# Kernel optimization log

Measured on AMD Instinct MI355X. Metric: run time of the kernel, lower is better.

The kernel has to match this reference:

```python
import jax, jax.numpy as jnp
import numpy as np

B, L, T = 32, 512, 48
START_ID, END_ID = 46, 47


def setup_inputs() -> dict:
    key = jax.random.key(0)
    kf, kt, ks = jax.random.split(key, 3)
    features = jax.random.normal(kf, (B, L, T), dtype=jnp.float32)
    transitions = jax.random.normal(kt, (T, T), dtype=jnp.float32) * 0.1
    seqLens = jax.random.randint(ks, (B,), 1, L + 1)  # lengths in [1, L]
    mask = jnp.arange(L)[None, :] < seqLens[:, None]  # [B, L] bool
    return {"features": features, "transitions": transitions,
            "seqLens": seqLens, "mask": mask}


def reference(features, transitions, seqLens, mask):
    # features: [B, L, T]; transitions: [T, T]
    Bv, Lv, Tv = features.shape
    # scores[b, t, i, j] = transitions[i, j] + features[b, t, i]
    scores = transitions[None, None, :, :] + features[:, :, :, None]  # [B,L,T,T]

    alpha0 = scores[:, 0, :, START_ID]  # [B, T] = trans[:, start] + feat[:, 0, :]

    def step(alpha_prev, s_t):
        # alpha_t[b, i] = logsumexp_j( alpha_{t-1}[b, j] + s_t[b, i, j] )
        a = jax.nn.logsumexp(alpha_prev[:, None, :] + s_t, axis=2)
        return a, a

    scores_t = jnp.swapaxes(scores, 0, 1)  # [L, B, T, T]
    _, alphas_rest = jax.lax.scan(step, alpha0, scores_t[1:])  # [L-1, B, T]
    alpha = jnp.concatenate([alpha0[None], alphas_rest], axis=0)  # [L, B, T]
    alpha = jnp.swapaxes(alpha, 0, 1)  # [B, L, T]

    # gather alpha at position seqLens-1 per batch element
    last = jnp.take_along_axis(alpha, (seqLens - 1)[:, None, None], axis=1)[:, 0, :]  # [B,T]
    last = last + transitions[END_ID][None, :]
    logZ = jnp.sum(jax.nn.logsumexp(last, axis=1))  # scalar
    return logZ, scores
```

## Files before the change

kernel.cpp:

```cpp
#include <hip/hip_runtime.h>

#define BB 32
#define LL 512
#define TT 48
#define START_ID 46
#define END_ID 47

constexpr int   BLT  = BB * LL * TT;
constexpr unsigned NSC = 37748736u;
constexpr unsigned NGRP = 9437183u;

constexpr int SEGS   = 31;
constexpr int SEGLEN = 16;
constexpr int GW     = 1152;
constexpr int NSEG   = BB * SEGS;
constexpr int SOFF   = NSEG * GW;
constexpr int ZOFF   = SOFF + NSEG;
constexpr int ZFOFF  = ZOFF + 32;
constexpr size_t WS_NEED = (size_t)(ZFOFF + 32) * 4;

typedef __fp16 f16x2 __attribute__((ext_vector_type(2)));
typedef __fp16 f16x8 __attribute__((ext_vector_type(8)));
typedef float  f32x4 __attribute__((ext_vector_type(4)));
typedef unsigned u32x4 __attribute__((ext_vector_type(4)));

__device__ __forceinline__ float fexp2(float x) { return __builtin_amdgcn_exp2f(x); }
__device__ __forceinline__ float flog2(float x) { return __builtin_amdgcn_logf(x); }
__device__ __forceinline__ float rfirst(float x) {
  return __uint_as_float(__builtin_amdgcn_readfirstlane(__float_as_uint(x)));
}
__device__ __forceinline__ float fdot2(f16x2 a, f16x2 b, float c) {
  return __builtin_amdgcn_fdot2(a, b, c, false);
}
__device__ __forceinline__ f16x2 bc(unsigned u) { return __builtin_bit_cast(f16x2, u); }
__device__ __forceinline__ unsigned pk2(float a, float b) {
  return __builtin_bit_cast(unsigned, __builtin_amdgcn_cvt_pkrtz(a, b));
}
__device__ __forceinline__ float dpp_xor1(float x) {
  return __int_as_float(__builtin_amdgcn_update_dpp(
      __float_as_int(x), __float_as_int(x), 0xB1, 0xF, 0xF, true));
}
__device__ __forceinline__ f16x8 b8(unsigned d0, unsigned d1) {
  u32x4 u; u.x = d0; u.y = d1; u.z = 0u; u.w = 0u;
  return __builtin_bit_cast(f16x8, u);
}
__device__ __forceinline__ f32x4 MF(f16x8 a, f16x8 b, f32x4 c) {
  return __builtin_amdgcn_mfma_f32_16x16x32_f16(a, b, c, 0, 0, 0);
}
__device__ __forceinline__ unsigned magicv(unsigned i) {
  return 0x5EC0DE5Au + i * 2654435761u;
}

#define GLD16(gp, lp)                                                        \
  __builtin_amdgcn_global_load_lds(                                          \
      (const __attribute__((address_space(1))) unsigned int*)(gp),           \
      (__attribute__((address_space(3))) unsigned int*)(lp), 16, 0, 0)

__device__ __attribute__((noinline)) void crf_tree_body(
    const float* __restrict__ feat, const float* __restrict__ trans,
    float* __restrict__ ws, float* lds, int wg, int lane)
{
  constexpr float LOG2E = 1.4426950408889634f;
  unsigned* gws = (unsigned*)ws;
  const int b  = wg / SEGS, s = wg - b * SEGS;
  const int col = lane & 15, grp = lane >> 4, rb = grp * 4;

  const char* gbase = (const char*)feat + (size_t)b * 98304 + (size_t)(SEGLEN * s + 1) * 192;
#pragma unroll
  for (int w = 0; w < 3; ++w)
    GLD16(gbase + w * 1024 + lane * 16, (char*)lds + w * 1024);

  float4 T_[3][3];
#pragma unroll
  for (int I = 0; I < 3; ++I)
#pragma unroll
    for (int K = 0; K < 3; ++K) {
      const float4 t4 = *(const float4*)(trans + (I * 16 + col) * 48 + K * 16 + rb);
      T_[I][K].x = fexp2(t4.x * LOG2E);
      T_[I][K].y = fexp2(t4.y * LOG2E);
      T_[I][K].z = fexp2(t4.z * LOG2E);
      T_[I][K].w = fexp2(t4.w * LOG2E);
    }

  unsigned Bd[3][3][2];
#pragma unroll
  for (int K = 0; K < 3; ++K)
#pragma unroll
    for (int J = 0; J < 3; ++J) {
      const float b0 = (K == J && rb + 0 == col) ? 1.f : 0.f;
      const float b1 = (K == J && rb + 1 == col) ? 1.f : 0.f;
      const float b2 = (K == J && rb + 2 == col) ? 1.f : 0.f;
      const float b3 = (K == J && rb + 3 == col) ? 1.f : 0.f;
      Bd[K][J][0] = pk2(b0, b1);
      Bd[K][J][1] = pk2(b2, b3);
    }

  asm volatile("s_waitcnt vmcnt(0)" ::: "memory");
  __builtin_amdgcn_sched_barrier(0);

  float km = 0.f, Sacc = 0.f;
  f32x4 C[3][3];
  const f32x4 zz = {0.f, 0.f, 0.f, 0.f};

  for (int p = 0; p < SEGLEN; ++p) {
    Sacc += km;
    float ef[3];
    ef[0] = fexp2(fmaf(lds[p * 48 +  0 + col], LOG2E, -km));
    ef[1] = fexp2(fmaf(lds[p * 48 + 16 + col], LOG2E, -km));
    ef[2] = fexp2(fmaf(lds[p * 48 + 32 + col], LOG2E, -km));
    f16x8 A_[3][3];
#pragma unroll
    for (int I = 0; I < 3; ++I)
#pragma unroll
      for (int K = 0; K < 3; ++K) {
        u32x4 u;
        u.x = pk2(T_[I][K].x * ef[I], T_[I][K].y * ef[I]);
        u.y = pk2(T_[I][K].z * ef[I], T_[I][K].w * ef[I]);
        u.z = 0u; u.w = 0u;
        A_[I][K] = __builtin_bit_cast(f16x8, u);
      }
#pragma unroll
    for (int I = 0; I < 3; ++I)
#pragma unroll
      for (int J = 0; J < 3; ++J) {
        f32x4 c = MF(A_[I][0], b8(Bd[0][J][0], Bd[0][J][1]), zz);
        c = MF(A_[I][1], b8(Bd[1][J][0], Bd[1][J][1]), c);
        c = MF(A_[I][2], b8(Bd[2][J][0], Bd[2][J][1]), c);
        C[I][J] = c;
      }
    const unsigned u00 = __builtin_amdgcn_readfirstlane(__float_as_uint(C[0][0][0]));
    km = (float)((int)((u00 >> 23) & 255u) - 127);
#pragma unroll
    for (int K = 0; K < 3; ++K)
#pragma unroll
      for (int J = 0; J < 3; ++J) {
        Bd[K][J][0] = pk2(C[K][J][0], C[K][J][1]);
        Bd[K][J][1] = pk2(C[K][J][2], C[K][J][3]);
      }
  }

  const unsigned gb = (unsigned)wg * GW;
#pragma unroll
  for (int I = 0; I < 3; ++I)
#pragma unroll
    for (int J = 0; J < 3; ++J)
#pragma unroll
      for (int r = 0; r < 4; ++r) {
        const float cn = dpp_xor1(C[I][J][r]);
        const unsigned pk = pk2(C[I][J][r], cn);
        if (!(col & 1))
          gws[gb + (unsigned)((I * 16 + rb + r) * 24 + ((J * 16 + col) >> 1))] = pk;
      }
  if (lane == 0) ws[SOFF + wg] = Sacc;
}

__global__ __launch_bounds__(64) void crf_tree_kernel(
    const float* __restrict__ feat, const float* __restrict__ trans,
    float* __restrict__ ws)
{
  __shared__ __align__(16) float fls[SEGLEN * 48];
  crf_tree_body(feat, trans, ws, fls, blockIdx.x, threadIdx.x);
}

__device__ __attribute__((noinline)) void crf_phaseB(
    const float* __restrict__ feat, const float* __restrict__ trans,
    const int* __restrict__ seqLens, float* __restrict__ ws, int b, int lane)
{
  constexpr float LOG2E = 1.4426950408889634f;
  constexpr float LN2   = 0.6931471805599453f;
  const unsigned* gws = (const unsigned*)ws;
  const int ii = lane < 47 ? lane : 47;
  const int Lb = seqLens[b];
  const int steps = Lb - 1;
  const int nfull = steps >> 4;

  f16x2 E00,E01,E02,E03,E04,E05,E06,E07,E08,E09,E10,E11,
        E12,E13,E14,E15,E16,E17,E18,E19,E20,E21,E22,E23;
#define LDE(V, J) { const float e0_ = fexp2(trans[ii*48 + 2*(J)]     * LOG2E); \
                    const float e1_ = fexp2(trans[ii*48 + 2*(J) + 1] * LOG2E); \
                    V = __builtin_amdgcn_cvt_pkrtz(e0_, e1_); }
  LDE(E00,0)  LDE(E01,1)  LDE(E02,2)  LDE(E03,3)  LDE(E04,4)  LDE(E05,5)
  LDE(E06,6)  LDE(E07,7)  LDE(E08,8)  LDE(E09,9)  LDE(E10,10) LDE(E11,11)
  LDE(E12,12) LDE(E13,13) LDE(E14,14) LDE(E15,15) LDE(E16,16) LDE(E17,17)
  LDE(E18,18) LDE(E19,19) LDE(E20,20) LDE(E21,21) LDE(E22,22) LDE(E23,23)
#undef LDE
  const float tS = trans[ii * 48 + START_ID];
  const float tE = trans[END_ID * 48 + ii];
  const float* fb = feat + (size_t)b * (LL * TT);

  const float a0 = (tS + fb[ii]) * LOG2E;
  const float anch = rfirst(a0);
  float v = fexp2(a0 - anch);
  float sigma = anch;

#define RL24                                                               \
        unsigned s00,s01,s02,s03,s04,s05,s06,s07,s08,s09,s10,s11,          \
                 s12,s13,s14,s15,s16,s17,s18,s19,s20,s21,s22,s23;          \
        s00=__builtin_amdgcn_readlane(pku,0);  s01=__builtin_amdgcn_readlane(pku,2);  \
        s02=__builtin_amdgcn_readlane(pku,4);  s03=__builtin_amdgcn_readlane(pku,6);  \
        s04=__builtin_amdgcn_readlane(pku,8);  s05=__builtin_amdgcn_readlane(pku,10); \
        s06=__builtin_amdgcn_readlane(pku,12); s07=__builtin_amdgcn_readlane(pku,14); \
        s08=__builtin_amdgcn_readlane(pku,16); s09=__builtin_amdgcn_readlane(pku,18); \
        s10=__builtin_amdgcn_readlane(pku,20); s11=__builtin_amdgcn_readlane(pku,22); \
        s12=__builtin_amdgcn_readlane(pku,24); s13=__builtin_amdgcn_readlane(pku,26); \
        s14=__builtin_amdgcn_readlane(pku,28); s15=__builtin_amdgcn_readlane(pku,30); \
        s16=__builtin_amdgcn_readlane(pku,32); s17=__builtin_amdgcn_readlane(pku,34); \
        s18=__builtin_amdgcn_readlane(pku,36); s19=__builtin_amdgcn_readlane(pku,38); \
        s20=__builtin_amdgcn_readlane(pku,40); s21=__builtin_amdgcn_readlane(pku,42); \
        s22=__builtin_amdgcn_readlane(pku,44); s23=__builtin_amdgcn_readlane(pku,46);

  const unsigned* grow = gws + (size_t)(b * SEGS) * GW + ii * 24;
  u32x4 h0,h1,h2,h3,h4,h5, n0,n1,n2,n3,n4,n5;
  if (nfull > 0) {
    const u32x4* gp = (const u32x4*)grow;
    h0 = gp[0]; h1 = gp[1]; h2 = gp[2]; h3 = gp[3]; h4 = gp[4]; h5 = gp[5];
  }
  for (int s = 0; s < nfull; ++s) {
    if (s + 1 < nfull) {
      const u32x4* gp = (const u32x4*)(grow + (size_t)(s + 1) * GW);
      n0 = gp[0]; n1 = gp[1]; n2 = gp[2]; n3 = gp[3]; n4 = gp[4]; n5 = gp[5];
    }
    const float pn = dpp_xor1(v);
    const unsigned pku = pk2(v, pn);
    RL24
    float d0, d1, d2, d3;
    d0 = fdot2(bc(h0.x), bc(s00), 0.0f);
    d1 = fdot2(bc(h0.y), bc(s01), 0.0f);
    d2 = fdot2(bc(h0.z), bc(s02), 0.0f);
    d3 = fdot2(bc(h0.w), bc(s03), 0.0f);
    d0 = fdot2(bc(h1.x), bc(s04), d0);
    d1 = fdot2(bc(h1.y), bc(s05), d1);
    d2 = fdot2(bc(h1.z), bc(s06), d2);
    d3 = fdot2(bc(h1.w), bc(s07), d3);
    d0 = fdot2(bc(h2.x), bc(s08), d0);
    d1 = fdot2(bc(h2.y), bc(s09), d1);
    d2 = fdot2(bc(h2.z), bc(s10), d2);
    d3 = fdot2(bc(h2.w), bc(s11), d3);
    d0 = fdot2(bc(h3.x), bc(s12), d0);
    d1 = fdot2(bc(h3.y), bc(s13), d1);
    d2 = fdot2(bc(h3.z), bc(s14), d2);
    d3 = fdot2(bc(h3.w), bc(s15), d3);
    d0 = fdot2(bc(h4.x), bc(s16), d0);
    d1 = fdot2(bc(h4.y), bc(s17), d1);
    d2 = fdot2(bc(h4.z), bc(s18), d2);
    d3 = fdot2(bc(h4.w), bc(s19), d3);
    d0 = fdot2(bc(h5.x), bc(s20), d0);
    d1 = fdot2(bc(h5.y), bc(s21), d1);
    d2 = fdot2(bc(h5.z), bc(s22), d2);
    d3 = fdot2(bc(h5.w), bc(s23), d3);
    const float dot = (d0 + d1) + (d2 + d3);
    const unsigned ub = __builtin_amdgcn_readfirstlane(__float_as_uint(dot));
    const int e = (int)((ub >> 23) & 255u) - 127;
    v = dot * __uint_as_float((unsigned)(127 - e) << 23);
    sigma += (float)e + ws[SOFF + b * SEGS + s];
    h0 = n0; h1 = n1; h2 = n2; h3 = n3; h4 = n4; h5 = n5;
  }

  int t = nfull * 16 + 1;
  if (t <= steps) {
    float f_cur = fb[(size_t)t * 48 + ii];
    for (; t <= steps; ++t) {
      const int tn = (t + 1 <= steps) ? t + 1 : t;
      const float f_nxt = fb[(size_t)tn * 48 + ii];
      const float pn = dpp_xor1(v);
      const unsigned pku = pk2(v, pn);
      RL24
      float d0, d1, d2, d3;
      d0 = fdot2(E00, bc(s00), 0.0f);
      d1 = fdot2(E01, bc(s01), 0.0f);
      d2 = fdot2(E02, bc(s02), 0.0f);
      d3 = fdot2(E03, bc(s03), 0.0f);
      d0 = fdot2(E04, bc(s04), d0);
      d1 = fdot2(E05, bc(s05), d1);
      d2 = fdot2(E06, bc(s06), d2);
      d3 = fdot2(E07, bc(s07), d3);
      d0 = fdot2(E08, bc(s08), d0);
      d1 = fdot2(E09, bc(s09), d1);
      d2 = fdot2(E10, bc(s10), d2);
      d3 = fdot2(E11, bc(s11), d3);
      d0 = fdot2(E12, bc(s12), d0);
      d1 = fdot2(E13, bc(s13), d1);
      d2 = fdot2(E14, bc(s14), d2);
      d3 = fdot2(E15, bc(s15), d3);
      d0 = fdot2(E16, bc(s16), d0);
      d1 = fdot2(E17, bc(s17), d1);
      d2 = fdot2(E18, bc(s18), d2);
      d3 = fdot2(E19, bc(s19), d3);
      d0 = fdot2(E20, bc(s20), d0);
      d1 = fdot2(E21, bc(s21), d1);
      d2 = fdot2(E22, bc(s22), d2);
      d3 = fdot2(E23, bc(s23), d3);
      const float dot = (d0 + d1) + (d2 + d3);
      const float w = dot * fexp2(f_cur * LOG2E);
      const unsigned ub = __builtin_amdgcn_readfirstlane(__float_as_uint(w));
      const int e = (int)((ub >> 23) & 255u) - 127;
      v = w * __uint_as_float((unsigned)(127 - e) << 23);
      sigma += (float)e;
      f_cur = f_nxt;
    }
  }
#undef RL24

  float contrib = (lane < 48) ? v * fexp2(tE * LOG2E) : 0.0f;
#pragma unroll
  for (int off = 32; off; off >>= 1) contrib += __shfl_xor(contrib, off, 64);
  if (lane == 0) ws[ZOFF + b] = (flog2(contrib) + sigma) * LN2;
  __threadfence();
  if (lane == 0)
    __hip_atomic_store((unsigned*)ws + ZFOFF + b, magicv((unsigned)(NSEG + b)),
                       __ATOMIC_RELAXED, __HIP_MEMORY_SCOPE_AGENT);
}

__device__ __forceinline__ void scores_writer_rng(
    const float* __restrict__ feat, float* __restrict__ out,
    float* lds, unsigned k, unsigned kstride, unsigned kend)
{
  for (; k < kend; k += kstride) {
    const unsigned idx = 3u + 4u * k;
    const unsigned r0 = idx / 48u;
    const unsigned j0 = idx - r0 * 48u;
    const unsigned i0 = r0 % 48u;
    const unsigned rn = (r0 + 1u < (unsigned)BLT) ? r0 + 1u : (unsigned)(BLT - 1);
    const float fa = feat[r0];
    const float fn = feat[rn];
    const unsigned i1 = (i0 + 1u < 48u) ? i0 + 1u : 0u;
    float v[4];
#pragma unroll
    for (int e = 0; e < 4; ++e) {
      const unsigned j = j0 + (unsigned)e;
      const bool wr = j >= 48u;
      const unsigned jj = wr ? j - 48u : j;
      v[e] = (wr ? fn : fa) + lds[(wr ? i1 : i0) * 48u + jj];
    }
    float4 o; o.x = v[0]; o.y = v[1]; o.z = v[2]; o.w = v[3];
    *(float4*)(out + 4u + 4u * (size_t)k) = o;
  }
}

__global__ __launch_bounds__(256) void crf_fusedB_kernel(
    const float* __restrict__ feat, const float* __restrict__ trans,
    const int* __restrict__ seqLens, float* __restrict__ out,
    float* __restrict__ ws)
{
  __shared__ __align__(16) float lds[2304];
  const int blk = blockIdx.x;
  const int tid = threadIdx.x;

  if (blk < BB) {
    const int b = blk;
    if (tid >= 64) {
      if (b == 0) {
        if (tid <= 66) out[tid - 63] = feat[0] + trans[tid - 64];
        else if (tid == 67) out[NSC] = feat[BLT - 1] + trans[2303];
      }
      return;
    }
    crf_phaseB(feat, trans, seqLens, ws, b, tid);
    if (b == 0) {
      const unsigned* zf = (const unsigned*)ws + ZFOFF;
      if (tid > 0 && tid < 32) {
        const unsigned want = magicv((unsigned)(NSEG + tid));
        while (__hip_atomic_load(zf + tid, __ATOMIC_RELAXED, __HIP_MEMORY_SCOPE_AGENT) != want)
          __builtin_amdgcn_s_sleep(2);
      }
      __threadfence();
      float v = (tid < 32) ? ws[ZOFF + tid] : 0.0f;
#pragma unroll
      for (int off = 32; off; off >>= 1) v += __shfl_xor(v, off, 64);
      if (tid == 0) out[0] = v;
    }
    return;
  }

  for (int s = tid; s < 2304; s += 256) lds[s] = trans[s];
  __syncthreads();
  scores_writer_rng(feat, out, lds,
                    (unsigned)(blk - BB) * 256u + tid,
                    (gridDim.x - BB) * 256u, NGRP);
}

__device__ __attribute__((noinline)) void crf_recursion_body(
    const float* __restrict__ feat, const float* __restrict__ trans,
    const int* __restrict__ seqLens, float* __restrict__ ws,
    float* lds, int blk, int lane)
{
  constexpr float LOG2E = 1.4426950408889634f;
  const int ii = lane < 47 ? lane : 47;
  const char* gbase = (const char*)(feat + (size_t)blk * (LL * TT));
  const int Lb = seqLens[blk];

#pragma unroll
  for (int w = 0; w < 6; ++w)
    GLD16(gbase + w * 1024 + lane * 16, (char*)&lds[0] + w * 1024);

  f16x2 E00,E01,E02,E03,E04,E05,E06,E07,E08,E09,E10,E11,
        E12,E13,E14,E15,E16,E17,E18,E19,E20,E21,E22,E23;
#define LDE(V, J) { const float e0_ = fexp2(trans[ii*48 + 2*(J)]     * LOG2E); \
                    const float e1_ = fexp2(trans[ii*48 + 2*(J) + 1] * LOG2E); \
                    V = __builtin_amdgcn_cvt_pkrtz(e0_, e1_); }
  LDE(E00,0)  LDE(E01,1)  LDE(E02,2)  LDE(E03,3)  LDE(E04,4)  LDE(E05,5)
  LDE(E06,6)  LDE(E07,7)  LDE(E08,8)  LDE(E09,9)  LDE(E10,10) LDE(E11,11)
  LDE(E12,12) LDE(E13,13) LDE(E14,14) LDE(E15,15) LDE(E16,16) LDE(E17,17)
  LDE(E18,18) LDE(E19,19) LDE(E20,20) LDE(E21,21) LDE(E22,22) LDE(E23,23)
#undef LDE
  const float tS = trans[ii * 48 + START_ID];
  const float tE = trans[END_ID * 48 + ii];

  asm volatile("s_waitcnt vmcnt(0)" ::: "memory");
  __builtin_amdgcn_sched_barrier(0);

  const float f00 = lds[ii];
  float a2 = (tS + f00) * LOG2E;
  float M2 = rfirst(a2) + 5.0f;

  const int nch = (Lb + 31) >> 5;
  for (int c = 0; c < nch; ++c) {
    const bool pre = (c + 1 < nch);
    if (pre) {
      const char* g = gbase + (size_t)(c + 1) * 6144;
      char* l = (char*)&lds[((c + 1) & 1) * 1536];
#pragma unroll
      for (int w = 0; w < 6; ++w) GLD16(g + w * 1024 + lane * 16, l + w * 1024);
    }
    const int tend = ((c + 1) * 32 < Lb) ? (c + 1) * 32 : Lb;
    const int t0 = (c == 0 ? 1 : c * 32);
    const int base = (c & 1) * 1536 + ii;
    if (t0 < tend) {
      float f_cur = lds[base + (t0 - c * 32) * 48];
      for (int t = t0; t < tend; ++t) {
        const int lnxt = ((t + 1 < tend) ? t + 1 : t) - c * 32;
        const float f_nxt = lds[base + lnxt * 48];
        const float p  = fexp2(a2 - M2);
        const float pn = dpp_xor1(p);
        const unsigned pku = pk2(p, pn);
        unsigned s00,s01,s02,s03,s04,s05,s06,s07,s08,s09,s10,s11,
                 s12,s13,s14,s15,s16,s17,s18,s19,s20,s21,s22,s23;
#define RL(K) __builtin_amdgcn_readlane(pku, (K))
        s00=RL(0);  s01=RL(2);  s02=RL(4);  s03=RL(6);
        s04=RL(8);  s05=RL(10); s06=RL(12); s07=RL(14);
        s08=RL(16); s09=RL(18); s10=RL(20); s11=RL(22);
        s12=RL(24); s13=RL(26); s14=RL(28); s15=RL(30);
        s16=RL(32); s17=RL(34); s18=RL(36); s19=RL(38);
        s20=RL(40); s21=RL(42); s22=RL(44); s23=RL(46);
#undef RL
        float d0, d1, d2, d3;
        d0 = fdot2(E00, bc(s00), 0.0f);
        d1 = fdot2(E01, bc(s01), 0.0f);
        d2 = fdot2(E02, bc(s02), 0.0f);
        d3 = fdot2(E03, bc(s03), 0.0f);
        d0 = fdot2(E04, bc(s04), d0);
        d1 = fdot2(E05, bc(s05), d1);
        d2 = fdot2(E06, bc(s06), d2);
        d3 = fdot2(E07, bc(s07), d3);
        d0 = fdot2(E08, bc(s08), d0);
        d1 = fdot2(E09, bc(s09), d1);
        d2 = fdot2(E10, bc(s10), d2);
        d3 = fdot2(E11, bc(s11), d3);
        d0 = fdot2(E12, bc(s12), d0);
        d1 = fdot2(E13, bc(s13), d1);
        d2 = fdot2(E14, bc(s14), d2);
        d3 = fdot2(E15, bc(s15), d3);
        d0 = fdot2(E16, bc(s16), d0);
        d1 = fdot2(E17, bc(s17), d1);
        d2 = fdot2(E18, bc(s18), d2);
        d3 = fdot2(E19, bc(s19), d3);
        d0 = fdot2(E20, bc(s20), d0);
        d1 = fdot2(E21, bc(s21), d1);
        d2 = fdot2(E22, bc(s22), d2);
        d3 = fdot2(E23, bc(s23), d3);
        const float dot = (d0 + d1) + (d2 + d3);
        a2 = fmaf(f_cur, LOG2E, M2 + flog2(dot));
        M2 = rfirst(a2) + 5.0f;
        f_cur = f_nxt;
      }
    }
    asm volatile("s_waitcnt vmcnt(0)" ::: "memory");
    __builtin_amdgcn_sched_barrier(0);
  }

  float last2 = (lane < 48) ? (a2 + tE * LOG2E) : -3.0e38f;
  float m2 = last2;
#pragma unroll
  for (int off = 32; off; off >>= 1) m2 = fmaxf(m2, __shfl_xor(m2, off, 64));
  float e = (lane < 48) ? fexp2(last2 - m2) : 0.0f;
#pragma unroll
  for (int off = 32; off; off >>= 1) e += __shfl_xor(e, off, 64);
  if (lane == 0) ws[blk] = (m2 + flog2(e)) * 0.6931471805599453f;
}

__global__ __launch_bounds__(256) void crf_fused2_kernel(
    const float* __restrict__ feat, const float* __restrict__ trans,
    const int* __restrict__ seqLens, float* __restrict__ out,
    float* __restrict__ ws)
{
  __shared__ __align__(16) float lds[3072];
  const int blk = blockIdx.x;
  if (blk < BB) {
    if (threadIdx.x >= 64) return;
    crf_recursion_body(feat, trans, seqLens, ws, lds, blk, threadIdx.x);
    return;
  }
  for (int s = threadIdx.x; s < 2304; s += 256) lds[s] = trans[s];
  __syncthreads();
  scores_writer_rng(feat, out, lds,
                    (unsigned)(blk - BB) * 256u + threadIdx.x,
                    (gridDim.x - BB) * 256u, NGRP);
}

__global__ void crf_finalize_kernel(const float* __restrict__ feat,
                                    const float* __restrict__ trans,
                                    const float* __restrict__ zws,
                                    float* __restrict__ out)
{
  const int t = threadIdx.x;
  float v = (t < 32) ? zws[t] : 0.0f;
#pragma unroll
  for (int off = 32; off; off >>= 1) v += __shfl_xor(v, off, 64);
  if (t == 0) out[0] = v;
  else if (t <= 3) out[t] = feat[0] + trans[t - 1];
  else if (t == 4) out[NSC] = feat[BLT - 1] + trans[2303];
}

extern "C" void kernel_launch(void* const* d_in, const int* in_sizes, int n_in,
                              void* d_out, int out_size, void* d_ws, size_t ws_size,
                              hipStream_t stream) {
  const float* feat    = (const float*)d_in[0];
  const float* trans   = (const float*)d_in[1];
  const int*   seqLens = (const int*)d_in[2];
  float* out = (float*)d_out;
  float* ws  = (float*)d_ws;

  if (ws_size >= WS_NEED) {
    hipLaunchKernelGGL(crf_tree_kernel, dim3(NSEG), dim3(64), 0, stream,
                       feat, trans, ws);
    hipLaunchKernelGGL(crf_fusedB_kernel, dim3(2048), dim3(256), 0, stream,
                       feat, trans, seqLens, out, ws);
  } else {
    hipLaunchKernelGGL(crf_fused2_kernel, dim3(2048), dim3(256), 0, stream,
                       feat, trans, seqLens, out, ws);
    hipLaunchKernelGGL(crf_finalize_kernel, dim3(1), dim3(64), 0, stream,
                       feat, trans, ws, out);
  }
}
```

Measured before the change: 66.04 us.

## Run tree and phase-B in one cooperative kernel, then write scores separately

Merges the segment-tree pass and the per-batch phase-B recursion into a single cooperative kernel separated by a grid-wide sync. The score-tensor writer becomes its own kernel, with one extra block that does the final logZ reduction and the boundary elements. This removes the flag-polling spin-wait on magic values. In exchange, the serial phase-B recursion no longer overlaps with the large scores write, which now runs only after the cooperative kernel finishes. It also adds grid.sync overhead and a cooperative launch.

New measurement: 182.0 us. 2.76x slower.

```diff
diff --git a/kernel.cpp b/kernel.cpp
--- a/kernel.cpp
+++ b/kernel.cpp
@@ -1,4 +1,5 @@
 #include <hip/hip_runtime.h>
+#include <hip/hip_cooperative_groups.h>
 
 #define BB 32
 #define LL 512
@@ -16,8 +17,9 @@
 constexpr int NSEG   = BB * SEGS;
 constexpr int SOFF   = NSEG * GW;
 constexpr int ZOFF   = SOFF + NSEG;
-constexpr int ZFOFF  = ZOFF + 32;
-constexpr size_t WS_NEED = (size_t)(ZFOFF + 32) * 4;
+constexpr size_t WS_NEED = (size_t)(ZOFF + 32) * 4;
+
+constexpr int NB_WRITE = 2048;
 
 typedef __fp16 f16x2 __attribute__((ext_vector_type(2)));
 typedef __fp16 f16x8 __attribute__((ext_vector_type(8)));
@@ -46,9 +48,6 @@
 }
 __device__ __forceinline__ f32x4 MF(f16x8 a, f16x8 b, f32x4 c) {
   return __builtin_amdgcn_mfma_f32_16x16x32_f16(a, b, c, 0, 0, 0);
-}
-__device__ __forceinline__ unsigned magicv(unsigned i) {
-  return 0x5EC0DE5Au + i * 2654435761u;
 }
 
 #define GLD16(gp, lp)                                                        \
@@ -305,10 +304,17 @@
 #pragma unroll
   for (int off = 32; off; off >>= 1) contrib += __shfl_xor(contrib, off, 64);
   if (lane == 0) ws[ZOFF + b] = (flog2(contrib) + sigma) * LN2;
-  __threadfence();
-  if (lane == 0)
-    __hip_atomic_store((unsigned*)ws + ZFOFF + b, magicv((unsigned)(NSEG + b)),
-                       __ATOMIC_RELAXED, __HIP_MEMORY_SCOPE_AGENT);
+}
+
+__global__ __launch_bounds__(64) void crf_coop_kernel(
+    const float* __restrict__ feat, const float* __restrict__ trans,
+    const int* __restrict__ seqLens, float* __restrict__ ws)
+{
+  __shared__ __align__(16) float fls[SEGLEN * 48];
+  crf_tree_body(feat, trans, ws, fls, blockIdx.x, threadIdx.x);
+  cooperative_groups::this_grid().sync();
+  if (blockIdx.x < BB)
+    crf_phaseB(feat, trans, seqLens, ws, blockIdx.x, threadIdx.x);
 }
 
 __device__ __forceinline__ void scores_writer_rng(
@@ -337,46 +343,63 @@
   }
 }
 
-__global__ __launch_bounds__(256) void crf_fusedB_kernel(
-    const float* __restrict__ feat, const float* __restrict__ trans,
-    const int* __restrict__ seqLens, float* __restrict__ out,
-    float* __restrict__ ws)
+__global__ __launch_bounds__(256) void crf_writer_kernel(
+    const float* __restrict__ feat, const float* __restrict__ trans,
+    const float* __restrict__ ws, float* __restrict__ out)
 {
   __shared__ __align__(16) float lds[2304];
   const int blk = blockIdx.x;
   const int tid = threadIdx.x;
 
-  if (blk < BB) {
-    const int b = blk;
-    if (tid >= 64) {
-      if (b == 0) {
-        if (tid <= 66) out[tid - 63] = feat[0] + trans[tid - 64];
-        else if (tid == 67) out[NSC] = feat[BLT - 1] + trans[2303];
-      }
-      return;
-    }
-    crf_phaseB(feat, trans, seqLens, ws, b, tid);
-    if (b == 0) {
-      const unsigned* zf = (const unsigned*)ws + ZFOFF;
-      if (tid > 0 && tid < 32) {
-        const unsigned want = magicv((unsigned)(NSEG + tid));
-        while (__hip_atomic_load(zf + tid, __ATOMIC_RELAXED, __HIP_MEMORY_SCOPE_AGENT) != want)
-          __builtin_amdgcn_s_sleep(2);
-      }
-      __threadfence();
-      float v = (tid < 32) ? ws[ZOFF + tid] : 0.0f;
-#pragma unroll
-      for (int off = 32; off; off >>= 1) v += __shfl_xor(v, off, 64);
-      if (tid == 0) out[0] = v;
-    }
+  if (blk == NB_WRITE) {
+    if (tid >= 64) return;
+    float v = (tid < 32) ? ws[ZOFF + tid] : 0.0f;
+#pragma unroll
+    for (int off = 32; off; off >>= 1) v += __shfl_xor(v, off, 64);
+    if (tid == 0) out[0] = v;
+    else if (tid <= 3) out[tid] = feat[0] + trans[tid - 1];
+    else if (tid == 4) out[NSC] = feat[BLT - 1] + trans[2303];
     return;
   }
 
   for (int s = tid; s < 2304; s += 256) lds[s] = trans[s];
   __syncthreads();
   scores_writer_rng(feat, out, lds,
-                    (unsigned)(blk - BB) * 256u + tid,
+                    (unsigned)blk * 256u + tid,
+                    (unsigned)NB_WRITE * 256u, NGRP);
+}
+
+__global__ __launch_bounds__(256) void crf_fusedB_kernel(
+    const float* __restrict__ feat, const float* __restrict__ trans,
+    const int* __restrict__ seqLens, float* __restrict__ out,
+    float* __restrict__ ws)
+{
+  __shared__ __align__(16) float lds[2304];
+  const int blk = blockIdx.x;
+  if (blk < BB) {
+    if (threadIdx.x >= 64) return;
+    crf_phaseB(feat, trans, seqLens, ws, blk, threadIdx.x);
+    return;
+  }
+  for (int s = threadIdx.x; s < 2304; s += 256) lds[s] = trans[s];
+  __syncthreads();
+  scores_writer_rng(feat, out, lds,
+                    (unsigned)(blk - BB) * 256u + threadIdx.x,
                     (gridDim.x - BB) * 256u, NGRP);
+}
+
+__global__ void crf_finalize_kernel(const float* __restrict__ feat,
+                                    const float* __restrict__ trans,
+                                    const float* __restrict__ zws,
+                                    float* __restrict__ out)
+{
+  const int t = threadIdx.x;
+  float v = (t < 32) ? zws[t] : 0.0f;
+#pragma unroll
+  for (int off = 32; off; off >>= 1) v += __shfl_xor(v, off, 64);
+  if (t == 0) out[0] = v;
+  else if (t <= 3) out[t] = feat[0] + trans[t - 1];
+  else if (t == 4) out[NSC] = feat[BLT - 1] + trans[2303];
 }
 
 __device__ __attribute__((noinline)) void crf_recursion_body(
@@ -507,20 +530,6 @@
                     (gridDim.x - BB) * 256u, NGRP);
 }
 
-__global__ void crf_finalize_kernel(const float* __restrict__ feat,
-                                    const float* __restrict__ trans,
-                                    const float* __restrict__ zws,
-                                    float* __restrict__ out)
-{
-  const int t = threadIdx.x;
-  float v = (t < 32) ? zws[t] : 0.0f;
-#pragma unroll
-  for (int off = 32; off; off >>= 1) v += __shfl_xor(v, off, 64);
-  if (t == 0) out[0] = v;
-  else if (t <= 3) out[t] = feat[0] + trans[t - 1];
-  else if (t == 4) out[NSC] = feat[BLT - 1] + trans[2303];
-}
-
 extern "C" void kernel_launch(void* const* d_in, const int* in_sizes, int n_in,
                               void* d_out, int out_size, void* d_ws, size_t ws_size,
                               hipStream_t stream) {
@@ -530,11 +539,29 @@
   float* out = (float*)d_out;
   float* ws  = (float*)d_ws;
 
-  if (ws_size >= WS_NEED) {
+  static int coop_ok = -1;
+  if (coop_ok < 0) {
+    int dev = 0;
+    (void)hipGetDevice(&dev);
+    int v = 0;
+    if (hipDeviceGetAttribute(&v, hipDeviceAttributeCooperativeLaunch, dev) != hipSuccess)
+      v = 0;
+    coop_ok = v;
+  }
+
+  if (ws_size >= WS_NEED && coop_ok) {
+    void* a1[] = {(void*)&feat, (void*)&trans, (void*)&seqLens, (void*)&ws};
+    hipLaunchCooperativeKernel((const void*)crf_coop_kernel, dim3(NSEG), dim3(64),
+                               a1, 0, stream);
+    hipLaunchKernelGGL(crf_writer_kernel, dim3(NB_WRITE + 1), dim3(256), 0, stream,
+                       feat, trans, ws, out);
+  } else if (ws_size >= WS_NEED) {
     hipLaunchKernelGGL(crf_tree_kernel, dim3(NSEG), dim3(64), 0, stream,
                        feat, trans, ws);
     hipLaunchKernelGGL(crf_fusedB_kernel, dim3(2048), dim3(256), 0, stream,
                        feat, trans, seqLens, out, ws);
+    hipLaunchKernelGGL(crf_finalize_kernel, dim3(1), dim3(64), 0, stream,
+                       feat, trans, ws + ZOFF, out);
   } else {
     hipLaunchKernelGGL(crf_fused2_kernel, dim3(2048), dim3(256), 0, stream,
                        feat, trans, seqLens, out, ws);
```
